# Optimization experiments

Measured on AMD Instinct MI355X. Metric: run time of the kernel, lower is better.

The kernel has to match this reference:

```python
import jax, jax.numpy as jnp
import numpy as np

H = 16          # query heads
KV = 8          # kv heads
D = 256         # head_dim
HID = 3584      # hidden_size
ROPE_BASE = 10000.0
SCALING = 256.0 ** -0.5          # query_pre_attn_scalar ** -0.5
SOFTCAP = 50.0                   # attn_logit_softcapping
WINDOW = 1536 - 1                # sliding_window - 1 (layer_idx 0 is even)


def _rope_neox(x, positions):
    # x: [T, nh, D]; neox style: rotate the two halves of the head dim
    half = D // 2
    inv_freq = 1.0 / (ROPE_BASE ** (jnp.arange(0, D, 2, dtype=jnp.float32) / D))  # [half]
    freqs = positions.astype(jnp.float32)[:, None] * inv_freq[None, :]            # [T, half]
    cos = jnp.cos(freqs)[:, None, :]  # [T, 1, half]
    sin = jnp.sin(freqs)[:, None, :]
    x1, x2 = x[..., :half], x[..., half:]
    return jnp.concatenate([x1 * cos - x2 * sin, x2 * cos + x1 * sin], axis=-1)


def setup_inputs() -> dict:
    key = jax.random.key(0)
    k1, k2, k3 = jax.random.split(key, 3)
    T = 3072
    hidden_states = jax.random.normal(k1, (T, HID), dtype=jnp.float32)
    w_qkv = jax.random.normal(k2, (H * D + 2 * KV * D, HID), dtype=jnp.float32) * 0.02
    w_o = jax.random.normal(k3, (HID, H * D), dtype=jnp.float32) * 0.02
    positions = jnp.arange(T, dtype=jnp.int64)
    return {"positions": positions, "hidden_states": hidden_states,
            "w_qkv": w_qkv, "w_o": w_o}


def reference(positions, hidden_states, w_qkv, w_o):
    T = hidden_states.shape[0]
    qkv = hidden_states @ w_qkv.T                       # [T, (H+2KV)*D]
    q, k, v = jnp.split(qkv, [H * D, H * D + KV * D], axis=-1)
    q = q.reshape(T, H, D)
    k = k.reshape(T, KV, D)
    v = v.reshape(T, KV, D)
    q = _rope_neox(q, positions)
    k = _rope_neox(k, positions)
    # GQA: repeat kv heads (2 query heads per kv head)
    k = jnp.repeat(k, H // KV, axis=1)                  # [T, H, D]
    v = jnp.repeat(v, H // KV, axis=1)
    scores = jnp.einsum('thd,shd->hts', q, k) * SCALING  # [H, T, T]
    scores = SOFTCAP * jnp.tanh(scores / SOFTCAP)       # logit softcapping
    i = positions[:, None]
    j = positions[None, :]
    mask = (j <= i) & (i - j <= WINDOW)                 # causal + sliding window
    scores = jnp.where(mask[None, :, :], scores, -jnp.inf)
    probs = jax.nn.softmax(scores, axis=-1)
    attn = jnp.einsum('hts,shd->thd', probs, v).reshape(T, H * D)
    return attn @ w_o.T                                 # [T, HID]
```

## Files before the change

### kernel.cpp

```cpp
#include <hip/hip_runtime.h>
#include <math.h>

typedef unsigned short u16;
typedef __attribute__((ext_vector_type(8))) short short8;
typedef __attribute__((ext_vector_type(4))) float f32x4;
typedef __attribute__((ext_vector_type(4))) unsigned short u16x4;

#define HN 16
#define KVH 8
#define DH 256
#define HID 3584
#define T_LEN 3072
#define QKV_N 8192
#define O_N 4096
#define WIN 1535
#define SCALING 0.0625f
#define SOFTCAP 50.0f
#define KOFF 4096
#define VOFF 6144
#define PSTR 72
#define NJT 48
#define M_FIX 20.0f

__device__ __forceinline__ u16 f2bf(float f) {
  unsigned u = __float_as_uint(f);
  u += 0x7FFFu + ((u >> 16) & 1u);
  return (u16)(u >> 16);
}
__device__ __forceinline__ float bf2f(u16 b) {
  return __uint_as_float(((unsigned)b) << 16);
}

__device__ __forceinline__ void gload_lds16(const void* g, void* l) {
  __builtin_amdgcn_global_load_lds(
      (const __attribute__((address_space(1))) void*)g,
      (__attribute__((address_space(3))) void*)l, 16, 0, 0);
}

__device__ __forceinline__ f32x4 mfma_bf16(short8 a, short8 b, f32x4 c) {
  return __builtin_amdgcn_mfma_f32_16x16x32_bf16(a, b, c, 0, 0, 0);
}

__global__ __launch_bounds__(256) void cvt_kernel(const float* __restrict__ in,
                                                  u16* __restrict__ out, int n) {
  int i = (blockIdx.x * 256 + threadIdx.x) * 4;
  if (i >= n) return;
  float4 v = *(const float4*)(in + i);
  u16x4 o;
  o[0] = f2bf(v.x); o[1] = f2bf(v.y); o[2] = f2bf(v.z); o[3] = f2bf(v.w);
  *(u16x4*)(out + i) = o;
}

template <int OUT_BF16>
__global__ __launch_bounds__(512, 2) void gemm8(const u16* __restrict__ A,
                                                const u16* __restrict__ B,
                                                void* __restrict__ Cv,
                                                int N, int K, int ntn, int cpx) {
  __shared__ u16 sA[2][256 * 64];
  __shared__ u16 sB[2][256 * 64];

  const int bid = blockIdx.x;
  const int wg = (bid & 7) * cpx + (bid >> 3);
  const int bm = wg / ntn, bn = wg % ntn;
  const int row0 = bm * 256, col0 = bn * 256;
  const int tid = threadIdx.x, lane = tid & 63, wid = tid >> 6;
  const int wr = wid >> 2, wc = wid & 3;

  const int srow = lane >> 3;
  const int sg = (lane & 7) ^ srow;
  const u16* Asrc = A + (size_t)(row0 + wid * 32 + srow) * K + sg * 8;
  const u16* Bsrc = B + (size_t)(col0 + wid * 32 + srow) * K + sg * 8;
  const size_t rK8 = (size_t)8 * K;

  f32x4 acc[8][4] = {};
  const int NT = K >> 6;

#pragma unroll
  for (int i = 0; i < 4; ++i) {
    gload_lds16(Asrc + i * rK8, &sA[0][(wid * 4 + i) * 512]);
    gload_lds16(Bsrc + i * rK8, &sB[0][(wid * 4 + i) * 512]);
  }

  const int fr = lane & 15;
  const int g0 = (lane >> 4) ^ (lane & 7);
  const int g1 = (4 + (lane >> 4)) ^ (lane & 7);

  for (int t = 0; t < NT; ++t) {
    const int d = t & 1;
    if (t + 1 < NT) {
      const u16* As = Asrc + (size_t)(t + 1) * 64;
      const u16* Bs = Bsrc + (size_t)(t + 1) * 64;
#pragma unroll
      for (int i = 0; i < 4; ++i) {
        gload_lds16(As + i * rK8, &sA[d ^ 1][(wid * 4 + i) * 512]);
        gload_lds16(Bs + i * rK8, &sB[d ^ 1][(wid * 4 + i) * 512]);
      }
      __builtin_amdgcn_sched_barrier(0);
      asm volatile("s_waitcnt vmcnt(8)" ::: "memory");
    } else {
      asm volatile("s_waitcnt vmcnt(0)" ::: "memory");
    }
    __builtin_amdgcn_sched_barrier(0);
    __builtin_amdgcn_s_barrier();
    __builtin_amdgcn_sched_barrier(0);

    __builtin_amdgcn_s_setprio(1);
#pragma unroll
    for (int kk = 0; kk < 2; ++kk) {
      const int gk = kk ? g1 : g0;
      short8 af[8];
#pragma unroll
      for (int mi = 0; mi < 8; ++mi)
        af[mi] = *(const short8*)&sA[d][(wr * 128 + mi * 16 + fr) * 64 + gk * 8];
#pragma unroll
      for (int nh = 0; nh < 2; ++nh) {
        short8 bf[2];
#pragma unroll
        for (int nb = 0; nb < 2; ++nb)
          bf[nb] = *(const short8*)&sB[d][(wc * 64 + (nh * 2 + nb) * 16 + fr) * 64 + gk * 8];
#pragma unroll
        for (int mi = 0; mi < 8; ++mi)
#pragma unroll
          for (int nb = 0; nb < 2; ++nb)
            acc[mi][nh * 2 + nb] = mfma_bf16(af[mi], bf[nb], acc[mi][nh * 2 + nb]);
      }
    }
    __builtin_amdgcn_s_setprio(0);
    __builtin_amdgcn_sched_barrier(0);
    __builtin_amdgcn_s_barrier();
    __builtin_amdgcn_sched_barrier(0);
  }

#pragma unroll
  for (int mi = 0; mi < 8; ++mi) {
#pragma unroll
    for (int ni = 0; ni < 4; ++ni) {
      const int r = row0 + wr * 128 + mi * 16 + (lane >> 4) * 4;
      const int c = col0 + wc * 64 + ni * 16 + (lane & 15);
#pragma unroll
      for (int j = 0; j < 4; ++j) {
        float v = acc[mi][ni][j];
        if (OUT_BF16)
          ((u16*)Cv)[(size_t)(r + j) * N + c] = f2bf(v);
        else
          ((float*)Cv)[(size_t)(r + j) * N + c] = v;
      }
    }
  }
}

__global__ __launch_bounds__(256) void rope_kernel(u16* __restrict__ qkv) {
  int idx = blockIdx.x * 256 + threadIdx.x;
  int d = idx & 127;
  int hh = (idx >> 7) % 24;
  int t = idx / (24 * 128);
  if (t >= T_LEN) return;
  size_t base = (size_t)t * QKV_N + (hh < HN ? hh * DH : HN * DH + (hh - HN) * DH);
  float inv = exp2f((float)d * (-13.287712379549449f / 128.0f));
  float ang = (float)t * inv;
  float s = sinf(ang), c = cosf(ang);
  float x1 = bf2f(qkv[base + d]);
  float x2 = bf2f(qkv[base + d + 128]);
  qkv[base + d] = f2bf(x1 * c - x2 * s);
  qkv[base + d + 128] = f2bf(x2 * c + x1 * s);
}

__global__ __launch_bounds__(256) void vtrans_kernel(const u16* __restrict__ qkv,
                                                     u16* __restrict__ vt) {
  __shared__ u16 tile[256 * 72];
  const int jb = blockIdx.x * 64;
  const int kvh = blockIdx.y;
  const int tid = threadIdx.x;
  const int t = tid & 63, dc = tid >> 6;

  const u16* src = qkv + (size_t)(jb + t) * QKV_N + VOFF + kvh * DH + dc * 64;
#pragma unroll
  for (int i = 0; i < 8; ++i) {
    short8 v = *(const short8*)(src + i * 8);
    int d0 = dc * 64 + i * 8;
#pragma unroll
    for (int j = 0; j < 8; ++j) tile[(d0 + j) * 72 + t] = (u16)(short)v[j];
  }
  __syncthreads();

  u16* dst = vt + ((size_t)kvh * NJT + blockIdx.x) * 16384;
#pragma unroll
  for (int s = 0; s < 8; ++s) {
    int G = s * 256 + tid;
    int d = G >> 3, g = G & 7;
    short8 x = *(const short8*)&tile[d * 72 + ((g ^ (d & 7)) * 8)];
    *(short8*)(dst + G * 8) = x;
  }
}

__global__ __launch_bounds__(256) void attn_kernel(const u16* __restrict__ qkv,
                                                   const u16* __restrict__ vt,
                                                   u16* __restrict__ po,
                                                   float* __restrict__ ml) {
  const int wg = blockIdx.x;
  const int kvh = wg & 7;
  const int rest = wg >> 3;
  const int qt = rest >> 2;
  const int c = (rest >> 1) & 1;
  const int h = kvh * 2 + (rest & 1);
  const int qb = qt * 64;
  const int tid = threadIdx.x, lane = tid & 63, w = tid >> 6;

  __shared__ u16 sK[64 * 256];
  __shared__ u16 sVt[64 * 256];
  __shared__ u16 sP[4][16 * PSTR];

  int jmin = qb - WIN; if (jmin < 0) jmin = 0;
  const int jt0 = jmin >> 6, jt1 = qb >> 6;
  const int nt = jt1 - jt0 + 1;
  const int half = (nt + 1) >> 1;
  const int t_beg = (c == 0) ? jt0 : jt0 + half;
  const int t_end = (c == 0) ? jt0 + half : jt1 + 1;

  const int qrow = qb + w * 16 + (lane & 15);
  short8 qf[8];
  {
    const u16* qp = qkv + (size_t)qrow * QKV_N + h * DH + (lane >> 4) * 8;
#pragma unroll
    for (int kc = 0; kc < 8; ++kc) qf[kc] = *(const short8*)(qp + kc * 32);
  }

  f32x4 O[16];
#pragma unroll
  for (int i = 0; i < 16; ++i) O[i] = f32x4{0.f, 0.f, 0.f, 0.f};
  float lrow[4] = {0.f, 0.f, 0.f, 0.f};

  const int dl = lane & 15;
  const int vb0 = dl * 64 + (((lane >> 4)) ^ (dl & 7)) * 8;
  const int vb1 = dl * 64 + (((lane >> 4) + 4) ^ (dl & 7)) * 8;

  for (int jt = t_beg; jt < t_end; ++jt) {
    const int jb = jt * 64;
#pragma unroll
    for (int i = 0; i < 8; ++i) {
      int rl = w * 16 + i * 2 + (lane >> 5);
      int g = (lane & 31) ^ (rl & 7);
      gload_lds16(qkv + (size_t)(jb + rl) * QKV_N + KOFF + kvh * DH + g * 8,
                  &sK[(w * 16 + i * 2) * 256]);
    }
    {
      const u16* vtile = vt + ((size_t)kvh * NJT + jt) * 16384;
#pragma unroll
      for (int s = 0; s < 8; ++s) {
        int id = w * 8 + s;
        gload_lds16(vtile + id * 512 + lane * 8, &sVt[id * 512]);
      }
    }
    __syncthreads();

    f32x4 S[4];
#pragma unroll
    for (int nf = 0; nf < 4; ++nf) S[nf] = f32x4{0.f, 0.f, 0.f, 0.f};
#pragma unroll
    for (int nf = 0; nf < 4; ++nf) {
      int krow = nf * 16 + (lane & 15);
#pragma unroll
      for (int kc = 0; kc < 8; ++kc) {
        int g = (kc * 4 + (lane >> 4)) ^ (krow & 7);
        short8 kf = *(const short8*)&sK[krow * 256 + g * 8];
        S[nf] = mfma_bf16(qf[kc], kf, S[nf]);
      }
    }

#pragma unroll
    for (int r = 0; r < 4; ++r) {
      const int irow = qb + w * 16 + (lane >> 4) * 4 + r;
      const int ql = (lane >> 4) * 4 + r;
#pragma unroll
      for (int nf = 0; nf < 4; ++nf) {
        int j = jb + nf * 16 + (lane & 15);
        float x = S[nf][r] * (SCALING / SOFTCAP);
        float e2 = __expf(-2.0f * fabsf(x));
        float th = (1.0f - e2) / (1.0f + e2);
        th = x >= 0.0f ? th : -th;
        float val = SOFTCAP * th;
        bool ok = (j <= irow) && (irow - j <= WIN);
        float p = ok ? __expf(val - M_FIX) : 0.0f;
        lrow[r] += p;
        sP[w][ql * PSTR + nf * 16 + (lane & 15)] = f2bf(p);
      }
    }

    short8 pf0 = *(const short8*)&sP[w][(lane & 15) * PSTR + (lane >> 4) * 8];
    short8 pf1 = *(const short8*)&sP[w][(lane & 15) * PSTR + 32 + (lane >> 4) * 8];
#pragma unroll
    for (int nf = 0; nf < 16; ++nf) {
      short8 vf0 = *(const short8*)&sVt[nf * 1024 + vb0];
      short8 vf1 = *(const short8*)&sVt[nf * 1024 + vb1];
      O[nf] = mfma_bf16(pf0, vf0, O[nf]);
      O[nf] = mfma_bf16(pf1, vf1, O[nf]);
    }
    __syncthreads();
  }

#pragma unroll
  for (int r = 0; r < 4; ++r) {
#pragma unroll
    for (int off = 8; off >= 1; off >>= 1) lrow[r] += __shfl_xor(lrow[r], off);
  }

#pragma unroll
  for (int nf = 0; nf < 16; ++nf) {
    int d = nf * 16 + (lane & 15);
#pragma unroll
    for (int r = 0; r < 4; ++r) {
      int trow = qb + w * 16 + (lane >> 4) * 4 + r;
      po[(((size_t)c * T_LEN + trow) * HN + h) * DH + d] = f2bf(O[nf][r]);
    }
  }
  if ((lane & 15) == 0) {
#pragma unroll
    for (int r = 0; r < 4; ++r) {
      int trow = qb + w * 16 + (lane >> 4) * 4 + r;
      size_t mi = (((size_t)c * T_LEN + trow) * HN + h) * 2;
      ml[mi] = M_FIX;
      ml[mi + 1] = lrow[r];
    }
  }
}

__global__ __launch_bounds__(256) void combine_kernel(const u16* __restrict__ po,
                                                      const float* __restrict__ ml,
                                                      u16* __restrict__ attnb) {
  const int t = blockIdx.x;
  const int h = threadIdx.x >> 4;
  const int d0 = (threadIdx.x & 15) * 16;
  const size_t row = (size_t)t * HN + h;
  const float l0 = ml[row * 2 + 1];
  const float l1 = ml[(size_t)T_LEN * HN * 2 + row * 2 + 1];
  const float inv = 1.0f / (l0 + l1);
  const size_t i0 = row * DH + d0;
  const size_t i1 = (size_t)T_LEN * HN * DH + i0;
#pragma unroll
  for (int half = 0; half < 2; ++half) {
    short8 x0 = *(const short8*)(po + i0 + half * 8);
    short8 x1 = *(const short8*)(po + i1 + half * 8);
    short8 o;
#pragma unroll
    for (int j = 0; j < 8; ++j)
      o[j] = (short)f2bf((bf2f((u16)x0[j]) + bf2f((u16)x1[j])) * inv);
    *(short8*)(attnb + i0 + half * 8) = o;
  }
}

extern "C" void kernel_launch(void* const* d_in, const int* in_sizes, int n_in,
                              void* d_out, int out_size, void* d_ws, size_t ws_size,
                              hipStream_t stream) {
  const float* hidden = (const float*)d_in[1];
  const float* w_qkv = (const float*)d_in[2];
  const float* w_o = (const float*)d_in[3];
  float* out = (float*)d_out;
  char* ws = (char*)d_ws;

  u16* wqkvb = (u16*)(ws);
  u16* po = (u16*)(ws);
  float* ml = (float*)(ws + 50331648);
  u16* attnb = (u16*)(ws);
  u16* hb = (u16*)(ws + 58720256);
  u16* vtb = (u16*)(ws + 58720256);
  u16* qkvb = (u16*)(ws + 80740352);
  u16* wob = (u16*)(ws + 80740352);

  {
    int n = T_LEN * HID;
    cvt_kernel<<<dim3((n / 4 + 255) / 256), 256, 0, stream>>>(hidden, hb, n);
  }
  {
    int n = QKV_N * HID;
    cvt_kernel<<<dim3((n / 4 + 255) / 256), 256, 0, stream>>>(w_qkv, wqkvb, n);
  }
  gemm8<1><<<dim3(384), 512, 0, stream>>>(hb, wqkvb, qkvb, QKV_N, HID, 32, 48);
  {
    int n = T_LEN * 24 * 128;
    rope_kernel<<<dim3(n / 256), 256, 0, stream>>>(qkvb);
  }
  vtrans_kernel<<<dim3(NJT, KVH), 256, 0, stream>>>(qkvb, vtb);
  attn_kernel<<<dim3(1536), 256, 0, stream>>>(qkvb, vtb, po, ml);
  {
    int n = HID * O_N;
    cvt_kernel<<<dim3((n / 4 + 255) / 256), 256, 0, stream>>>(w_o, wob, n);
  }
  combine_kernel<<<dim3(T_LEN), 256, 0, stream>>>(po, ml, attnb);
  gemm8<0><<<dim3(168), 512, 0, stream>>>(attnb, wob, out, HID, O_N, 14, 21);
}
```

Measured before the change: 583.2 us.

## Halve GEMM K-tile to 32 and use 128-row tiles for output projection

```diff
diff --git a/kernel.cpp b/kernel.cpp
--- a/kernel.cpp
+++ b/kernel.cpp
@@ -51,52 +51,51 @@
   *(u16x4*)(out + i) = o;
 }
 
-template <int OUT_BF16>
-__global__ __launch_bounds__(512, 2) void gemm8(const u16* __restrict__ A,
+template <int OUT_BF16, int AFRAG>
+__global__ __launch_bounds__(512, 2) void gemmk(const u16* __restrict__ A,
                                                 const u16* __restrict__ B,
                                                 void* __restrict__ Cv,
                                                 int N, int K, int ntn, int cpx) {
-  __shared__ u16 sA[2][256 * 64];
-  __shared__ u16 sB[2][256 * 64];
+  const int BM = AFRAG * 32;
+  __shared__ u16 sA[2][AFRAG * 32 * 32];
+  __shared__ u16 sB[2][256 * 32];
 
   const int bid = blockIdx.x;
   const int wg = (bid & 7) * cpx + (bid >> 3);
   const int bm = wg / ntn, bn = wg % ntn;
-  const int row0 = bm * 256, col0 = bn * 256;
+  const int row0 = bm * BM, col0 = bn * 256;
   const int tid = threadIdx.x, lane = tid & 63, wid = tid >> 6;
   const int wr = wid >> 2, wc = wid & 3;
 
-  const int srow = lane >> 3;
-  const int sg = (lane & 7) ^ srow;
-  const u16* Asrc = A + (size_t)(row0 + wid * 32 + srow) * K + sg * 8;
+  const int srow = lane >> 2;
+  const int sg = (lane & 3) ^ ((lane >> 3) & 3);
+  const u16* Asrc = A + (size_t)(row0 + wid * (BM / 8) + srow) * K + sg * 8;
   const u16* Bsrc = B + (size_t)(col0 + wid * 32 + srow) * K + sg * 8;
-  const size_t rK8 = (size_t)8 * K;
-
-  f32x4 acc[8][4] = {};
-  const int NT = K >> 6;
-
-#pragma unroll
-  for (int i = 0; i < 4; ++i) {
-    gload_lds16(Asrc + i * rK8, &sA[0][(wid * 4 + i) * 512]);
-    gload_lds16(Bsrc + i * rK8, &sB[0][(wid * 4 + i) * 512]);
-  }
+  const size_t rK16 = (size_t)16 * K;
+
+  f32x4 acc[AFRAG][4] = {};
+  const int NT = K >> 5;
+
+  gload_lds16(Asrc, &sA[0][wid * (BM / 8) * 32]);
+  if (AFRAG == 8) gload_lds16(Asrc + rK16, &sA[0][(wid * (BM / 8) + 16) * 32]);
+  gload_lds16(Bsrc, &sB[0][wid * 32 * 32]);
+  gload_lds16(Bsrc + rK16, &sB[0][(wid * 32 + 16) * 32]);
 
   const int fr = lane & 15;
-  const int g0 = (lane >> 4) ^ (lane & 7);
-  const int g1 = (4 + (lane >> 4)) ^ (lane & 7);
+  const int gq = (lane >> 4) ^ ((fr >> 1) & 3);
 
   for (int t = 0; t < NT; ++t) {
     const int d = t & 1;
     if (t + 1 < NT) {
-      const u16* As = Asrc + (size_t)(t + 1) * 64;
-      const u16* Bs = Bsrc + (size_t)(t + 1) * 64;
-#pragma unroll
-      for (int i = 0; i < 4; ++i) {
-        gload_lds16(As + i * rK8, &sA[d ^ 1][(wid * 4 + i) * 512]);
-        gload_lds16(Bs + i * rK8, &sB[d ^ 1][(wid * 4 + i) * 512]);
-      }
+      const u16* As = Asrc + (size_t)(t + 1) * 32;
+      const u16* Bs = Bsrc + (size_t)(t + 1) * 32;
+      gload_lds16(As, &sA[d ^ 1][wid * (BM / 8) * 32]);
+      if (AFRAG == 8) gload_lds16(As + rK16, &sA[d ^ 1][(wid * (BM / 8) + 16) * 32]);
+      gload_lds16(Bs, &sB[d ^ 1][wid * 32 * 32]);
+      gload_lds16(Bs + rK16, &sB[d ^ 1][(wid * 32 + 16) * 32]);
       __builtin_amdgcn_sched_barrier(0);
-      asm volatile("s_waitcnt vmcnt(8)" ::: "memory");
+      if (AFRAG == 8) asm volatile("s_waitcnt vmcnt(4)" ::: "memory");
+      else            asm volatile("s_waitcnt vmcnt(3)" ::: "memory");
     } else {
       asm volatile("s_waitcnt vmcnt(0)" ::: "memory");
     }
@@ -105,25 +104,20 @@
     __builtin_amdgcn_sched_barrier(0);
 
     __builtin_amdgcn_s_setprio(1);
-#pragma unroll
-    for (int kk = 0; kk < 2; ++kk) {
-      const int gk = kk ? g1 : g0;
-      short8 af[8];
-#pragma unroll
-      for (int mi = 0; mi < 8; ++mi)
-        af[mi] = *(const short8*)&sA[d][(wr * 128 + mi * 16 + fr) * 64 + gk * 8];
-#pragma unroll
-      for (int nh = 0; nh < 2; ++nh) {
-        short8 bf[2];
-#pragma unroll
-        for (int nb = 0; nb < 2; ++nb)
-          bf[nb] = *(const short8*)&sB[d][(wc * 64 + (nh * 2 + nb) * 16 + fr) * 64 + gk * 8];
-#pragma unroll
-        for (int mi = 0; mi < 8; ++mi)
-#pragma unroll
-          for (int nb = 0; nb < 2; ++nb)
-            acc[mi][nh * 2 + nb] = mfma_bf16(af[mi], bf[nb], acc[mi][nh * 2 + nb]);
-      }
+    {
+      short8 af[AFRAG];
+#pragma unroll
+      for (int mi = 0; mi < AFRAG; ++mi)
+        af[mi] = *(const short8*)&sA[d][(wr * (BM / 2) + mi * 16 + fr) * 32 + gq * 8];
+      short8 bf[4];
+#pragma unroll
+      for (int ni = 0; ni < 4; ++ni)
+        bf[ni] = *(const short8*)&sB[d][(wc * 64 + ni * 16 + fr) * 32 + gq * 8];
+#pragma unroll
+      for (int mi = 0; mi < AFRAG; ++mi)
+#pragma unroll
+        for (int ni = 0; ni < 4; ++ni)
+          acc[mi][ni] = mfma_bf16(af[mi], bf[ni], acc[mi][ni]);
     }
     __builtin_amdgcn_s_setprio(0);
     __builtin_amdgcn_sched_barrier(0);
@@ -132,10 +126,10 @@
   }
 
 #pragma unroll
-  for (int mi = 0; mi < 8; ++mi) {
+  for (int mi = 0; mi < AFRAG; ++mi) {
 #pragma unroll
     for (int ni = 0; ni < 4; ++ni) {
-      const int r = row0 + wr * 128 + mi * 16 + (lane >> 4) * 4;
+      const int r = row0 + wr * (BM / 2) + mi * 16 + (lane >> 4) * 4;
       const int c = col0 + wc * 64 + ni * 16 + (lane & 15);
 #pragma unroll
       for (int j = 0; j < 4; ++j) {
@@ -374,7 +368,7 @@
     int n = QKV_N * HID;
     cvt_kernel<<<dim3((n / 4 + 255) / 256), 256, 0, stream>>>(w_qkv, wqkvb, n);
   }
-  gemm8<1><<<dim3(384), 512, 0, stream>>>(hb, wqkvb, qkvb, QKV_N, HID, 32, 48);
+  gemmk<1, 8><<<dim3(384), 512, 0, stream>>>(hb, wqkvb, qkvb, QKV_N, HID, 32, 48);
   {
     int n = T_LEN * 24 * 128;
     rope_kernel<<<dim3(n / 256), 256, 0, stream>>>(qkvb);
@@ -386,5 +380,5 @@
     cvt_kernel<<<dim3((n / 4 + 255) / 256), 256, 0, stream>>>(w_o, wob, n);
   }
   combine_kernel<<<dim3(T_LEN), 256, 0, stream>>>(po, ml, attnb);
-  gemm8<0><<<dim3(168), 512, 0, stream>>>(attnb, wob, out, HID, O_N, 14, 21);
-}
+  gemmk<0, 4><<<dim3(336), 512, 0, stream>>>(attnb, wob, out, HID, O_N, 14, 42);
+}
```

Result: slower. 651.8 us (+11.8%).

## Interleave GEMM global-to-LDS staging with MFMA phases in fine-grained pipeline

Applied to the files above, without the earlier changes.

```diff
diff --git a/kernel.cpp b/kernel.cpp
--- a/kernel.cpp
+++ b/kernel.cpp
@@ -41,6 +41,13 @@
   return __builtin_amdgcn_mfma_f32_16x16x32_bf16(a, b, c, 0, 0, 0);
 }
 
+#define BARX()                                  \
+  do {                                          \
+    __builtin_amdgcn_sched_barrier(0);          \
+    __builtin_amdgcn_s_barrier();               \
+    __builtin_amdgcn_sched_barrier(0);          \
+  } while (0)
+
 __global__ __launch_bounds__(256) void cvt_kernel(const float* __restrict__ in,
                                                   u16* __restrict__ out, int n) {
   int i = (blockIdx.x * 256 + threadIdx.x) * 4;
@@ -52,10 +59,10 @@
 }
 
 template <int OUT_BF16>
-__global__ __launch_bounds__(512, 2) void gemm8(const u16* __restrict__ A,
-                                                const u16* __restrict__ B,
-                                                void* __restrict__ Cv,
-                                                int N, int K, int ntn, int cpx) {
+__global__ __launch_bounds__(512, 2) void gemm8p(const u16* __restrict__ A,
+                                                 const u16* __restrict__ B,
+                                                 void* __restrict__ Cv,
+                                                 int N, int K, int ntn, int cpx) {
   __shared__ u16 sA[2][256 * 64];
   __shared__ u16 sB[2][256 * 64];
 
@@ -65,70 +72,94 @@
   const int row0 = bm * 256, col0 = bn * 256;
   const int tid = threadIdx.x, lane = tid & 63, wid = tid >> 6;
   const int wr = wid >> 2, wc = wid & 3;
+  const int NT = K >> 6;
 
   const int srow = lane >> 3;
   const int sg = (lane & 7) ^ srow;
-  const u16* Asrc = A + (size_t)(row0 + wid * 32 + srow) * K + sg * 8;
-  const u16* Bsrc = B + (size_t)(col0 + wid * 32 + srow) * K + sg * 8;
-  const size_t rK8 = (size_t)8 * K;
+
+  auto stage = [&](int tau, int kind) {
+    if (tau >= NT) return;
+    const int b = tau & 1;
+    const int rbase = (kind & 1) * 128;
+    const u16* src;
+    u16* dst;
+    if (kind >= 2) {
+      src = A + (size_t)(row0 + rbase + wid * 8 + srow) * K + (size_t)tau * 64 + sg * 8;
+      dst = &sA[b][(rbase + wid * 8) * 64];
+    } else {
+      src = B + (size_t)(col0 + rbase + wid * 8 + srow) * K + (size_t)tau * 64 + sg * 8;
+      dst = &sB[b][(rbase + wid * 8) * 64];
+    }
+    gload_lds16(src, dst);
+    gload_lds16(src + (size_t)64 * K, dst + 64 * 64);
+  };
 
   f32x4 acc[8][4] = {};
-  const int NT = K >> 6;
-
-#pragma unroll
-  for (int i = 0; i < 4; ++i) {
-    gload_lds16(Asrc + i * rK8, &sA[0][(wid * 4 + i) * 512]);
-    gload_lds16(Bsrc + i * rK8, &sB[0][(wid * 4 + i) * 512]);
-  }
-
   const int fr = lane & 15;
-  const int g0 = (lane >> 4) ^ (lane & 7);
-  const int g1 = (4 + (lane >> 4)) ^ (lane & 7);
-
-  for (int t = 0; t < NT; ++t) {
-    const int d = t & 1;
-    if (t + 1 < NT) {
-      const u16* As = Asrc + (size_t)(t + 1) * 64;
-      const u16* Bs = Bsrc + (size_t)(t + 1) * 64;
-#pragma unroll
-      for (int i = 0; i < 4; ++i) {
-        gload_lds16(As + i * rK8, &sA[d ^ 1][(wid * 4 + i) * 512]);
-        gload_lds16(Bs + i * rK8, &sB[d ^ 1][(wid * 4 + i) * 512]);
-      }
-      __builtin_amdgcn_sched_barrier(0);
-      asm volatile("s_waitcnt vmcnt(8)" ::: "memory");
+  const int fh = fr & 7;
+  const int gk0 = (lane >> 4) ^ fh;
+  const int gk1 = ((lane >> 4) + 4) ^ fh;
+
+  stage(0, 0); stage(0, 1); stage(0, 2); stage(0, 3);
+  stage(1, 0); stage(1, 1); stage(1, 2);
+  __builtin_amdgcn_sched_barrier(0);
+  asm volatile("s_waitcnt vmcnt(6)" ::: "memory");
+  BARX();
+
+  for (int u = 0; u < NT; ++u) {
+    const int b = u & 1;
+    const u16* pA = &sA[b][0];
+    const u16* pB = &sB[b][0];
+    short8 bf[4][2], afA[2][2], afB[2][2];
+
+#define LDB_(ni, kk) (*(const short8*)&pB[(wc * 64 + (ni)*16 + fr) * 64 + (kk ? gk1 : gk0) * 8])
+#define LDA_(mi, kk) (*(const short8*)&pA[(wr * 128 + (mi)*16 + fr) * 64 + (kk ? gk1 : gk0) * 8])
+#define MFMA2(AF, mi0)                                                   \
+  __builtin_amdgcn_s_setprio(1);                                        \
+  _Pragma("unroll") for (int ni = 0; ni < 4; ++ni) {                    \
+    acc[mi0][ni] = mfma_bf16(AF[0][0], bf[ni][0], acc[mi0][ni]);        \
+    acc[mi0][ni] = mfma_bf16(AF[0][1], bf[ni][1], acc[mi0][ni]);        \
+    acc[mi0 + 1][ni] = mfma_bf16(AF[1][0], bf[ni][0], acc[mi0 + 1][ni]);\
+    acc[mi0 + 1][ni] = mfma_bf16(AF[1][1], bf[ni][1], acc[mi0 + 1][ni]);\
+  }                                                                      \
+  __builtin_amdgcn_s_setprio(0);                                        \
+  asm volatile("s_waitcnt lgkmcnt(0)" ::: "memory");
+
+#pragma unroll
+    for (int ni = 0; ni < 4; ++ni) { bf[ni][0] = LDB_(ni, 0); bf[ni][1] = LDB_(ni, 1); }
+    afA[0][0] = LDA_(0, 0); afA[0][1] = LDA_(0, 1);
+    afA[1][0] = LDA_(1, 0); afA[1][1] = LDA_(1, 1);
+    stage(u + 1, 3);
+    BARX();
+    MFMA2(afA, 0);
+    BARX();
+    afA[0][0] = LDA_(2, 0); afA[0][1] = LDA_(2, 1);
+    afA[1][0] = LDA_(3, 0); afA[1][1] = LDA_(3, 1);
+    stage(u + 2, 0);
+    BARX();
+    MFMA2(afA, 2);
+    BARX();
+    afA[0][0] = LDA_(4, 0); afA[0][1] = LDA_(4, 1);
+    afA[1][0] = LDA_(5, 0); afA[1][1] = LDA_(5, 1);
+    afB[0][0] = LDA_(6, 0); afB[0][1] = LDA_(6, 1);
+    afB[1][0] = LDA_(7, 0); afB[1][1] = LDA_(7, 1);
+    stage(u + 2, 1);
+    BARX();
+    MFMA2(afA, 4);
+    BARX();
+    stage(u + 2, 2);
+    __builtin_amdgcn_sched_barrier(0);
+    if (u + 2 < NT) {
+      asm volatile("s_waitcnt vmcnt(6)" ::: "memory");
     } else {
       asm volatile("s_waitcnt vmcnt(0)" ::: "memory");
     }
-    __builtin_amdgcn_sched_barrier(0);
-    __builtin_amdgcn_s_barrier();
-    __builtin_amdgcn_sched_barrier(0);
-
-    __builtin_amdgcn_s_setprio(1);
-#pragma unroll
-    for (int kk = 0; kk < 2; ++kk) {
-      const int gk = kk ? g1 : g0;
-      short8 af[8];
-#pragma unroll
-      for (int mi = 0; mi < 8; ++mi)
-        af[mi] = *(const short8*)&sA[d][(wr * 128 + mi * 16 + fr) * 64 + gk * 8];
-#pragma unroll
-      for (int nh = 0; nh < 2; ++nh) {
-        short8 bf[2];
-#pragma unroll
-        for (int nb = 0; nb < 2; ++nb)
-          bf[nb] = *(const short8*)&sB[d][(wc * 64 + (nh * 2 + nb) * 16 + fr) * 64 + gk * 8];
-#pragma unroll
-        for (int mi = 0; mi < 8; ++mi)
-#pragma unroll
-          for (int nb = 0; nb < 2; ++nb)
-            acc[mi][nh * 2 + nb] = mfma_bf16(af[mi], bf[nb], acc[mi][nh * 2 + nb]);
-      }
-    }
-    __builtin_amdgcn_s_setprio(0);
-    __builtin_amdgcn_sched_barrier(0);
-    __builtin_amdgcn_s_barrier();
-    __builtin_amdgcn_sched_barrier(0);
+    BARX();
+    MFMA2(afB, 6);
+    BARX();
+#undef LDB_
+#undef LDA_
+#undef MFMA2
   }
 
 #pragma unroll
@@ -374,7 +405,7 @@
     int n = QKV_N * HID;
     cvt_kernel<<<dim3((n / 4 + 255) / 256), 256, 0, stream>>>(w_qkv, wqkvb, n);
   }
-  gemm8<1><<<dim3(384), 512, 0, stream>>>(hb, wqkvb, qkvb, QKV_N, HID, 32, 48);
+  gemm8p<1><<<dim3(384), 512, 0, stream>>>(hb, wqkvb, qkvb, QKV_N, HID, 32, 48);
   {
     int n = T_LEN * 24 * 128;
     rope_kernel<<<dim3(n / 256), 256, 0, stream>>>(qkvb);
@@ -386,5 +417,5 @@
     cvt_kernel<<<dim3((n / 4 + 255) / 256), 256, 0, stream>>>(w_o, wob, n);
   }
   combine_kernel<<<dim3(T_LEN), 256, 0, stream>>>(po, ml, attnb);
-  gemm8<0><<<dim3(168), 512, 0, stream>>>(attnb, wob, out, HID, O_N, 14, 21);
-}
+  gemm8p<0><<<dim3(168), 512, 0, stream>>>(attnb, wob, out, HID, O_N, 14, 21);
+}
```

Measured after the change: 555.4 us. 4.8% less time.
